# Performance work log

Measured on AMD Instinct MI355X. Metric: run time of the kernel, lower is better.

Reference implementation:

```python
import jax, jax.numpy as jnp
import numpy as np


def _gat_layer(h, mask, w, a_src, a_dst):
    # h: [B,C,N,Fin], w: [C,H,Fin,Fout], a_*: [C,H,Fout,1], mask: [B,N,N] (True where no edge)
    h_prime = jnp.einsum('bcni,chio->bchno', h, w)          # [B,C,H,N,Fout]
    t = jnp.tanh(h_prime)
    s = jnp.einsum('bchno,cho->bchn', t, a_src[..., 0])      # src scores
    d = jnp.einsum('bchno,cho->bchn', t, a_dst[..., 0])      # dst scores
    attn = s[..., :, None] + d[..., None, :]                 # [B,C,H,N,N]
    attn = jnp.where(attn >= 0, attn, 0.2 * attn)            # leaky_relu(0.2)
    attn = jnp.where(mask[:, None, None, :, :], jnp.float32(-1e12), attn)
    attn = jax.nn.softmax(attn, axis=-1)
    return jnp.einsum('bchnm,bchmo->bchno', attn, h_prime)   # [B,C,H,N,Fout]


def setup_inputs() -> dict:
    key = jax.random.key(0)
    ks = jax.random.split(key, 8)
    B, C, N, F0, H, F = 2, 2, 1024, 64, 8, 64

    def xavier(k, shape):
        fan_in, fan_out = shape[-2], shape[-1]
        lim = (6.0 / (fan_in + fan_out)) ** 0.5
        return jax.random.uniform(k, shape, jnp.float32, -lim, lim)

    x = jax.random.normal(ks[0], (B, C, N, F0), dtype=jnp.float32)
    adj = jax.random.randint(ks[1], (B, N, N), 0, 2, dtype=jnp.int32)
    w1 = xavier(ks[2], (C, H, F0, F))
    a_src1 = xavier(ks[3], (C, H, F, 1))
    a_dst1 = xavier(ks[4], (C, H, F, 1))
    w2 = xavier(ks[5], (C, H, H * F, F))
    a_src2 = xavier(ks[6], (C, H, F, 1))
    a_dst2 = xavier(ks[7], (C, H, F, 1))
    return {"x": x, "adj": adj, "w1": w1, "a_src1": a_src1, "a_dst1": a_dst1,
            "w2": w2, "a_src2": a_src2, "a_dst2": a_dst2}


def reference(x, adj, w1, a_src1, a_dst1, w2, a_src2, a_dst2):
    B, C, N, _ = x.shape
    adj_f = adj.astype(jnp.float32) + jnp.eye(N, dtype=jnp.float32)[None]  # add self-loops
    mask = adj_f == 0                                        # [B,N,N]
    out1 = _gat_layer(x, mask, w1, a_src1, a_dst1)           # [B,C,H,N,F]
    # permute heads next to features, flatten, elu (dropout is identity in eval)
    x1 = jax.nn.elu(jnp.transpose(out1, (0, 1, 3, 2, 4)).reshape(B, C, N, -1))
    out2 = _gat_layer(x1, mask, w2, a_src2, a_dst2)          # [B,C,H,N,F]
    return out2.mean(axis=2)                                 # mean over heads -> [B,C,N,F]
```

## Files before the change

kernel.cpp:

```cpp
#include <hip/hip_runtime.h>

#define BB 2
#define CC 2
#define NN 1024
#define HH 8
#define BCHN 32
#define SVN  (BCHN*NN)
#define LOG2E 1.44269504f

typedef _Float16 f16x8 __attribute__((ext_vector_type(8)));
typedef _Float16 f16x4 __attribute__((ext_vector_type(4)));
typedef __fp16 h16x2 __attribute__((ext_vector_type(2)));
typedef float f32x4 __attribute__((ext_vector_type(4)));

__device__ __forceinline__ float fexp2(float x) {
  float r; asm("v_exp_f32 %0, %1" : "=v"(r) : "v"(x)); return r;
}

__device__ __forceinline__ void gl_lds16(const _Float16* g, _Float16* l) {
  __builtin_amdgcn_global_load_lds(
      (const __attribute__((address_space(1))) void*)g,
      (__attribute__((address_space(3))) void*)l, 16, 0, 0);
}


__global__ __launch_bounds__(256) void proj1_fused(
    const float* __restrict__ x, const int* __restrict__ adj,
    const float* __restrict__ w1, const float* __restrict__ w2,
    const float* __restrict__ asrc, const float* __restrict__ adst,
    _Float16* __restrict__ w2T, unsigned long long* __restrict__ bmg,
    _Float16* __restrict__ HpT, float* __restrict__ s_out, float* __restrict__ d_out)
{
  __shared__ union {
    __align__(16) _Float16 tile[64*72];
    struct { float sp[4][32]; float sd[4][32]; } pr;
  } sm;
  const int bx = blockIdx.x;
  const int t = threadIdx.x;
  const int w = t >> 6, lane = t & 63;
  const int colr = lane & 15, quad = lane >> 4;

  if (bx < 1024) {
    const int bch = bx & 31;
    const int row0 = (bx >> 5) * 32;
    const int h = bch & 7; const int bc = bch >> 3; const int c = bc & 1;

    const float* Ar0 = x + ((size_t)bc*NN + row0 + colr)*64;
    const float* Ar1 = Ar0 + (size_t)16*64;
    const float* Bw  = w1 + ((size_t)(c*HH + h))*64*64 + w*16 + colr;

    f32x4 acc0 = {0.f,0.f,0.f,0.f}, acc1 = {0.f,0.f,0.f,0.f};
    #pragma unroll
    for (int kb = 0; kb < 64; kb += 32) {
      const float4 pa0 = *(const float4*)(Ar0 + kb + quad*8);
      const float4 pa1 = *(const float4*)(Ar0 + kb + quad*8 + 4);
      const float4 pb0 = *(const float4*)(Ar1 + kb + quad*8);
      const float4 pb1 = *(const float4*)(Ar1 + kb + quad*8 + 4);
      float bv[8];
      #pragma unroll
      for (int j = 0; j < 8; ++j) bv[j] = Bw[(size_t)(kb + quad*8 + j)*64];
      f16x8 a0, a1, bf;
      a0[0]=(_Float16)pa0.x; a0[1]=(_Float16)pa0.y; a0[2]=(_Float16)pa0.z; a0[3]=(_Float16)pa0.w;
      a0[4]=(_Float16)pa1.x; a0[5]=(_Float16)pa1.y; a0[6]=(_Float16)pa1.z; a0[7]=(_Float16)pa1.w;
      a1[0]=(_Float16)pb0.x; a1[1]=(_Float16)pb0.y; a1[2]=(_Float16)pb0.z; a1[3]=(_Float16)pb0.w;
      a1[4]=(_Float16)pb1.x; a1[5]=(_Float16)pb1.y; a1[6]=(_Float16)pb1.z; a1[7]=(_Float16)pb1.w;
      #pragma unroll
      for (int j = 0; j < 8; ++j) bf[j] = (_Float16)bv[j];
      acc0 = __builtin_amdgcn_mfma_f32_16x16x32_f16(a0, bf, acc0, 0, 0, 0);
      acc1 = __builtin_amdgcn_mfma_f32_16x16x32_f16(a1, bf, acc1, 0, 0, 0);
    }

    const float af  = asrc[(c*HH + h)*64 + w*16 + colr];
    const float bf_ = adst[(c*HH + h)*64 + w*16 + colr];
    _Float16* HT = HpT + (size_t)bch*65536 + (size_t)(row0 >> 5)*2048;

    #pragma unroll
    for (int mt = 0; mt < 2; ++mt) {
      const f32x4 a = mt ? acc1 : acc0;
      f16x4 hv;
      #pragma unroll
      for (int i = 0; i < 4; ++i) {
        const float v = a[i];
        hv[i] = (_Float16)v;
        const float ex = __expf(2.f*v);
        const float th = 1.f - 2.f/(ex + 1.f);
        float ps = th * af, pd = th * bf_;
        #pragma unroll
        for (int off = 1; off < 16; off <<= 1) {
          ps += __shfl_xor(ps, off);
          pd += __shfl_xor(pd, off);
        }
        if (colr == 0) {
          sm.pr.sp[w][mt*16 + quad*4 + i] = ps;
          sm.pr.sd[w][mt*16 + quad*4 + i] = pd;
        }
      }
      const int chunk = w*64 + (mt*2 + (quad >> 1))*16 + colr;
      *(f16x4*)(HT + chunk*8 + (quad & 1)*4) = hv;
    }
    __syncthreads();
    if (t < 32) {
      const float sv = sm.pr.sp[0][t] + sm.pr.sp[1][t] + sm.pr.sp[2][t] + sm.pr.sp[3][t];
      const float dv = sm.pr.sd[0][t] + sm.pr.sd[1][t] + sm.pr.sd[2][t] + sm.pr.sd[3][t];
      s_out[bch*NN + row0 + t] = sv * LOG2E;
      d_out[bch*NN + row0 + t] = dv * LOG2E;
    }
  } else if (bx < 1152) {
    const int u = bx - 1024;
    const int ch = u >> 3, k0 = (u & 7)*64;
    const float* src = w2 + ((size_t)ch*512 + k0)*64;
    #pragma unroll
    for (int j = 0; j < 4; ++j) {
      const int uu = t + j*256;
      const int k = uu >> 4, seg = uu & 15;
      const float4 v = ((const float4*)src)[(size_t)k*16 + seg];
      sm.tile[(seg*4+0)*72 + k] = (_Float16)v.x;
      sm.tile[(seg*4+1)*72 + k] = (_Float16)v.y;
      sm.tile[(seg*4+2)*72 + k] = (_Float16)v.z;
      sm.tile[(seg*4+3)*72 + k] = (_Float16)v.w;
    }
    __syncthreads();
    _Float16* dst = w2T + (size_t)ch*32768;
    #pragma unroll
    for (int j = 0; j < 2; ++j) {
      const int uu = t + j*256;
      const int f = uu >> 3, seg = uu & 7;
      const f16x8 o = *(const f16x8*)&sm.tile[f*72 + seg*8];
      const int kk = k0 + seg*8;
      const int chunk = (f >> 4)*64 + ((seg & 3))*16 + (f & 15);
      *(f16x8*)(dst + (size_t)(kk >> 5)*2048 + chunk*8) = o;
    }
  } else {
    const int g = (bx - 1152)*4 + w;
    const int base = g*32;
    #pragma unroll
    for (int jb = 0; jb < 4; ++jb) {
      int vals[8];
      #pragma unroll
      for (int i = 0; i < 8; ++i) {
        const int idx = base + jb*8 + i;
        const int b = idx >> 14;
        const int n = (idx >> 4) & (NN - 1);
        const int wd = idx & 15;
        vals[i] = adj[((size_t)b*NN + n)*NN + wd*64 + lane];
      }
      #pragma unroll
      for (int i = 0; i < 8; ++i) {
        const int idx = base + jb*8 + i;
        const int n = (idx >> 4) & (NN - 1);
        const int m = (idx & 15)*64 + lane;
        const unsigned long long bits = __ballot((vals[i] != 0) || (m == n));
        if (lane == 0) bmg[idx] = bits;
      }
    }
  }
}

template<int LAYER>
__global__ __launch_bounds__(256) void attn_coop(
    const _Float16* __restrict__ Hp, const float* __restrict__ s_arr,
    const float* __restrict__ d_arr, const unsigned long long* __restrict__ bmg,
    _Float16* __restrict__ outp)
{
  __shared__ struct {
    __align__(16) _Float16 stg[2][2048];
    __align__(16) float dstg[1024];
    float pw[4][16][68];
  } sm;
  const int bch = blockIdx.x;
  const int r0 = blockIdx.y * 64;
  const int t = threadIdx.x;
  const int wv = t >> 6, lane = t & 63;
  const int colr = lane & 15, quad = lane >> 4;
  const int b = bch >> 4;

  const float* dg = d_arr + (size_t)bch*NN;
  const float4* dg4 = (const float4*)dg;
  float mxl = -1e30f;
  #pragma unroll
  for (int j = 0; j < 4; ++j) {
    const float4 v = dg4[lane + 64*j];
    mxl = fmaxf(fmaxf(v.x, v.y), fmaxf(fmaxf(v.z, v.w), mxl));
  }
  #pragma unroll
  for (int off = 1; off < 64; off <<= 1) mxl = fmaxf(mxl, __shfl_xor(mxl, off));
  const float maxd = mxl;

  *(float4*)&sm.dstg[t*4] = dg4[t];

  const int r = r0 + wv*16 + colr;
  const float s = s_arr[(size_t)bch*NN + r];
  const float so = s + maxd;
  const float offs = fmaxf(so, 0.2f*so);
  const float sA = s - offs, sB = 0.2f*s - offs;

  unsigned long long m[16];
  {
    const unsigned long long* bm = bmg + ((size_t)b*NN + r)*16;
    #pragma unroll
    for (int j = 0; j < 16; ++j) m[j] = bm[j];
  }

  const _Float16* strip = Hp + (size_t)bch*65536;

  f32x4 acc[4];
  f32x4 accs = {0.f,0.f,0.f,0.f};
  #pragma unroll
  for (int ft = 0; ft < 4; ++ft) acc[ft] = (f32x4){0.f,0.f,0.f,0.f};
  f16x8 ones;
  #pragma unroll
  for (int i = 0; i < 8; ++i) ones[i] = (_Float16)1.f;

  asm volatile("s_waitcnt vmcnt(0) lgkmcnt(0)" ::: "memory");
  __builtin_amdgcn_s_barrier();

#define STAGE_T(tt) \
    gl_lds16(strip + (size_t)(tt)*2048 + wv*512 + lane*8, &sm.stg[(tt) & 1][wv*512]);

  STAGE_T(0);
  asm volatile("s_waitcnt vmcnt(0)" ::: "memory");
  __builtin_amdgcn_s_barrier();

  #pragma unroll 4
  for (int ks = 0; ks < 32; ++ks) {
    if (ks < 31) STAGE_T(ks + 1);

    f16x8 Bc[4];
    #pragma unroll
    for (int ft = 0; ft < 4; ++ft)
      Bc[ft] = *(const f16x8*)&sm.stg[ks & 1][ft*512 + lane*8];
    const float* dls = &sm.dstg[ks*32 + quad*8];
    const float4 da0 = *(const float4*)dls;
    const float4 da1 = *(const float4*)(dls + 4);
    asm volatile("s_waitcnt lgkmcnt(0)" ::: "memory");
    __builtin_amdgcn_sched_barrier(0);

    __builtin_amdgcn_s_setprio(1);
    const unsigned mb = (unsigned)((m[ks >> 1] >> ((ks & 1)*32 + quad*8)) & 0xFFull);
    const float dd[8] = {da0.x, da0.y, da0.z, da0.w, da1.x, da1.y, da1.z, da1.w};
    union { f16x8 v; h16x2 hh[4]; } A;
    #pragma unroll
    for (int jp = 0; jp < 4; ++jp) {
      float p[2];
      #pragma unroll
      for (int jj = 0; jj < 2; ++jj) {
        const int j = jp*2 + jj;
        const float dj = dd[j];
        const float l = fmaxf(sA + dj, fmaf(0.2f, dj, sB));
        p[jj] = ((mb >> j) & 1u) ? fexp2(l) : 0.f;
      }
      A.hh[jp] = __builtin_amdgcn_cvt_pkrtz(p[0], p[1]);
    }
    #pragma unroll
    for (int ft = 0; ft < 4; ++ft)
      acc[ft] = __builtin_amdgcn_mfma_f32_16x16x32_f16(A.v, Bc[ft], acc[ft], 0, 0, 0);
    accs = __builtin_amdgcn_mfma_f32_16x16x32_f16(A.v, ones, accs, 0, 0, 0);
    __builtin_amdgcn_s_setprio(0);

    if (ks < 31) asm volatile("s_waitcnt vmcnt(0)" ::: "memory");
    __builtin_amdgcn_s_barrier();
  }
#undef STAGE_T

  float inv[4];
  #pragma unroll
  for (int i = 0; i < 4; ++i) inv[i] = (LAYER == 2 ? 0.125f : 1.f) / accs[i];
  float (*pw)[68] = sm.pw[wv];
  #pragma unroll
  for (int ft = 0; ft < 4; ++ft)
    #pragma unroll
    for (int i = 0; i < 4; ++i)
      pw[quad*4 + i][ft*16 + colr] = acc[ft][i] * inv[i];
  const int row = lane >> 2, f0 = (lane & 3)*16;
  f16x8 o0, o1;
  #pragma unroll
  for (int j = 0; j < 8; ++j) {
    float v0 = pw[row][f0 + j];
    float v1 = pw[row][f0 + 8 + j];
    if (LAYER == 1) {
      v0 = v0 > 0.f ? v0 : expm1f(v0);
      v1 = v1 > 0.f ? v1 : expm1f(v1);
    }
    o0[j] = (_Float16)v0; o1[j] = (_Float16)v1;
  }
  const int rr = r0 + wv*16 + row;
  _Float16* dst;
  if (LAYER == 1) {
    const int bc = bch >> 3, h = bch & 7;
    dst = outp + ((size_t)bc*NN + rr)*512 + h*64 + f0;
  } else {
    dst = outp + ((size_t)bch*NN + rr)*64 + f0;
  }
  *(f16x8*)dst = o0;
  *(f16x8*)(dst + 8) = o1;
}

__global__ __launch_bounds__(256) void proj2_coop(
    const _Float16* __restrict__ x1, const _Float16* __restrict__ w2T,
    const float* __restrict__ asrc2, const float* __restrict__ adst2,
    _Float16* __restrict__ HpT2, float* __restrict__ s2, float* __restrict__ d2)
{
  __shared__ struct {
    __align__(16) _Float16 Ast[2][2048];
    __align__(16) _Float16 Bst[2][2048];
  } sm;
  const int bch = blockIdx.x;
  const int r0p = blockIdx.y * 64;
  const int t = threadIdx.x;
  const int wv = t >> 6, lane = t & 63;
  const int colr = lane & 15, quad = lane >> 4;
  const int h = bch & 7, bc = bch >> 3, c = bc & 1;

  const _Float16* Asrc = x1 + ((size_t)bc*NN + r0p + wv*16 + colr)*512 + quad*8;
  const _Float16* Bsrc = w2T + (size_t)(c*HH + h)*32768 + wv*512 + lane*8;

  f32x4 acc[4];
  #pragma unroll
  for (int ft = 0; ft < 4; ++ft) acc[ft] = (f32x4){0.f,0.f,0.f,0.f};

#define STAGE_P(tt) { \
    gl_lds16(Asrc + (tt)*32,           &sm.Ast[(tt) & 1][wv*512]); \
    gl_lds16(Bsrc + (size_t)(tt)*2048, &sm.Bst[(tt) & 1][wv*512]); }

  STAGE_P(0);
  asm volatile("s_waitcnt vmcnt(0)" ::: "memory");
  __builtin_amdgcn_s_barrier();

  #pragma unroll 4
  for (int ks = 0; ks < 16; ++ks) {
    if (ks < 15) STAGE_P(ks + 1);

    const f16x8 Af = *(const f16x8*)&sm.Ast[ks & 1][wv*512 + lane*8];
    f16x8 Bc[4];
    #pragma unroll
    for (int ft = 0; ft < 4; ++ft)
      Bc[ft] = *(const f16x8*)&sm.Bst[ks & 1][ft*512 + lane*8];
    asm volatile("s_waitcnt lgkmcnt(0)" ::: "memory");
    __builtin_amdgcn_sched_barrier(0);

    __builtin_amdgcn_s_setprio(1);
    #pragma unroll
    for (int ft = 0; ft < 4; ++ft)
      acc[ft] = __builtin_amdgcn_mfma_f32_16x16x32_f16(Af, Bc[ft], acc[ft], 0, 0, 0);
    __builtin_amdgcn_s_setprio(0);

    if (ks < 15) asm volatile("s_waitcnt vmcnt(0)" ::: "memory");
    __builtin_amdgcn_s_barrier();
  }
#undef STAGE_P

  float af[4], bfv[4];
  #pragma unroll
  for (int ft = 0; ft < 4; ++ft) {
    af[ft]  = asrc2[(c*HH + h)*64 + ft*16 + colr];
    bfv[ft] = adst2[(c*HH + h)*64 + ft*16 + colr];
  }
  #pragma unroll
  for (int i = 0; i < 4; ++i) {
    float ps = 0.f, pd = 0.f;
    #pragma unroll
    for (int ft = 0; ft < 4; ++ft) {
      const float v = acc[ft][i];
      const float ex = __expf(2.f*v);
      const float th = 1.f - 2.f/(ex + 1.f);
      ps += th * af[ft]; pd += th * bfv[ft];
    }
    #pragma unroll
    for (int off = 1; off < 16; off <<= 1) {
      ps += __shfl_xor(ps, off);
      pd += __shfl_xor(pd, off);
    }
    if (colr == 0) {
      s2[(size_t)bch*NN + r0p + wv*16 + quad*4 + i] = ps * LOG2E;
      d2[(size_t)bch*NN + r0p + wv*16 + quad*4 + i] = pd * LOG2E;
    }
  }
  _Float16* H2 = HpT2 + (size_t)bch*65536 + (size_t)((r0p >> 5) + (wv >> 1))*2048;
  const int cb = (wv & 1)*2 + (quad >> 1);
  #pragma unroll
  for (int ft = 0; ft < 4; ++ft) {
    f16x4 hv;
    #pragma unroll
    for (int i = 0; i < 4; ++i) hv[i] = (_Float16)acc[ft][i];
    const int chunk = ft*64 + cb*16 + colr;
    *(f16x4*)(H2 + chunk*8 + (quad & 1)*4) = hv;
  }
}

__global__ __launch_bounds__(256) void reduce_heads(
    const _Float16* __restrict__ out2, float* __restrict__ out)
{
  const int o = blockIdx.x*256 + threadIdx.x;
  const int f = o & 63;
  const int n = (o >> 6) & (NN - 1);
  const int bc = o >> 16;
  float acc = 0.f;
  #pragma unroll
  for (int h = 0; h < HH; ++h)
    acc += (float)out2[(((size_t)bc*HH + h)*NN + n)*64 + f];
  out[o] = acc;
}

extern "C" void kernel_launch(void* const* d_in, const int* in_sizes, int n_in,
                              void* d_out, int out_size, void* d_ws, size_t ws_size,
                              hipStream_t stream)
{
  const float* x   = (const float*)d_in[0];
  const int*   adj = (const int*)d_in[1];
  const float* w1  = (const float*)d_in[2];
  const float* as1 = (const float*)d_in[3];
  const float* ad1 = (const float*)d_in[4];
  const float* w2  = (const float*)d_in[5];
  const float* as2 = (const float*)d_in[6];
  const float* ad2 = (const float*)d_in[7];

  char* w8 = (char*)d_ws;
  _Float16* HpT  = (_Float16*)(w8);
  _Float16* HpT2 = (_Float16*)(w8 + (4u<<20));
  _Float16* w2T  = (_Float16*)(w8 + (8u<<20));
  float* s_v  = (float*)(w8 + (10u<<20));
  float* d_v  = (float*)(w8 + (10u<<20) + SVN*4);
  float* s2_v = (float*)(w8 + (10u<<20) + SVN*8);
  float* d2_v = (float*)(w8 + (10u<<20) + SVN*12);
  unsigned long long* bmg = (unsigned long long*)(w8 + (10u<<20) + SVN*16);
  _Float16* x1g = (_Float16*)(w8 + (16u<<20));
  _Float16* XB  = (_Float16*)(w8 + (20u<<20));

  proj1_fused<<<1408, 256, 0, stream>>>(x, adj, w1, w2, as1, ad1, w2T, bmg, HpT, s_v, d_v);
  attn_coop<1><<<dim3(BCHN, NN/64), 256, 0, stream>>>(HpT, s_v, d_v, bmg, x1g);
  proj2_coop<<<dim3(BCHN, NN/64), 256, 0, stream>>>(x1g, w2T, as2, ad2, HpT2, s2_v, d2_v);
  attn_coop<2><<<dim3(BCHN, NN/64), 256, 0, stream>>>(HpT2, s2_v, d2_v, bmg, XB);
  reduce_heads<<<dim3((unsigned)(out_size/256)), 256, 0, stream>>>(XB, (float*)d_out);
}
```

Before: 145.2 us.

## Fuse five kernel launches into one persistent kernel with grid barriers

Merges the projection, two attention passes, the second projection and the head reduction into a single persistent kernel of 512 blocks. Phases are separated by a software grid barrier built from atomic counters, which is reset with a memset before each launch. The aim is to remove per-launch overhead and the tail gaps between dependent kernels. In exchange it relies on all 512 blocks being co-resident (launch bounds of 2 blocks per CU) and adds atomic spin-wait cost. A timeout guard on the spin can break out before the barrier is reached, which risks incorrect results.

```diff
diff --git a/kernel.cpp b/kernel.cpp
--- a/kernel.cpp
+++ b/kernel.cpp
@@ -7,6 +7,7 @@
 #define BCHN 32
 #define SVN  (BCHN*NN)
 #define LOG2E 1.44269504f
+#define NBLK 512
 
 typedef _Float16 f16x8 __attribute__((ext_vector_type(8)));
 typedef _Float16 f16x4 __attribute__((ext_vector_type(4)));
@@ -23,26 +24,51 @@
       (__attribute__((address_space(3))) void*)l, 16, 0, 0);
 }
 
-
-__global__ __launch_bounds__(256) void proj1_fused(
-    const float* __restrict__ x, const int* __restrict__ adj,
+__device__ __forceinline__ void gbar(unsigned* cnt, unsigned* gen, unsigned g) {
+  __syncthreads();
+  if (threadIdx.x == 0) {
+    __threadfence();
+    if (atomicAdd(cnt, 1u) == g*(unsigned)NBLK - 1u) atomicAdd(gen, 1u);
+    int guard = 0;
+    while (__hip_atomic_load(gen, __ATOMIC_RELAXED, __HIP_MEMORY_SCOPE_AGENT) < g) {
+      __builtin_amdgcn_s_sleep(8);
+      if (++guard > (1 << 20)) break;
+    }
+    __threadfence();
+  }
+  __syncthreads();
+}
+
+
+union SmemU {
+  __align__(16) _Float16 tile[64*72];
+  struct { float sp[4][32]; float sd[4][32]; } pr;
+  struct {
+    __align__(16) _Float16 stg[2][2048];
+    __align__(16) float dstg[1024];
+    float pw[4][16][68];
+  } at;
+  struct {
+    __align__(16) _Float16 Ast[2][2048];
+    __align__(16) _Float16 Bst[2][2048];
+  } p2;
+};
+
+__device__ __forceinline__ void p1_unit(
+    int u, const float* __restrict__ x, const int* __restrict__ adj,
     const float* __restrict__ w1, const float* __restrict__ w2,
     const float* __restrict__ asrc, const float* __restrict__ adst,
     _Float16* __restrict__ w2T, unsigned long long* __restrict__ bmg,
-    _Float16* __restrict__ HpT, float* __restrict__ s_out, float* __restrict__ d_out)
+    _Float16* __restrict__ HpT, float* __restrict__ s_out, float* __restrict__ d_out,
+    SmemU& sm)
 {
-  __shared__ union {
-    __align__(16) _Float16 tile[64*72];
-    struct { float sp[4][32]; float sd[4][32]; } pr;
-  } sm;
-  const int bx = blockIdx.x;
   const int t = threadIdx.x;
   const int w = t >> 6, lane = t & 63;
   const int colr = lane & 15, quad = lane >> 4;
 
-  if (bx < 1024) {
-    const int bch = bx & 31;
-    const int row0 = (bx >> 5) * 32;
+  if (u < 1024) {
+    const int bch = u & 31;
+    const int row0 = (u >> 5) * 32;
     const int h = bch & 7; const int bc = bch >> 3; const int c = bc & 1;
 
     const float* Ar0 = x + ((size_t)bc*NN + row0 + colr)*64;
@@ -105,9 +131,9 @@
       s_out[bch*NN + row0 + t] = sv * LOG2E;
       d_out[bch*NN + row0 + t] = dv * LOG2E;
     }
-  } else if (bx < 1152) {
-    const int u = bx - 1024;
-    const int ch = u >> 3, k0 = (u & 7)*64;
+  } else if (u < 1152) {
+    const int uu0 = u - 1024;
+    const int ch = uu0 >> 3, k0 = (uu0 & 7)*64;
     const float* src = w2 + ((size_t)ch*512 + k0)*64;
     #pragma unroll
     for (int j = 0; j < 4; ++j) {
@@ -130,8 +156,8 @@
       const int chunk = (f >> 4)*64 + ((seg & 3))*16 + (f & 15);
       *(f16x8*)(dst + (size_t)(kk >> 5)*2048 + chunk*8) = o;
     }
-  } else {
-    const int g = (bx - 1152)*4 + w;
+  } else if (u < 1408) {
+    const int g = (u - 1152)*4 + w;
     const int base = g*32;
     #pragma unroll
     for (int jb = 0; jb < 4; ++jb) {
@@ -157,18 +183,13 @@
 }
 
 template<int LAYER>
-__global__ __launch_bounds__(256) void attn_coop(
-    const _Float16* __restrict__ Hp, const float* __restrict__ s_arr,
+__device__ __forceinline__ void attn_phase(
+    int bid, const _Float16* __restrict__ Hp, const float* __restrict__ s_arr,
     const float* __restrict__ d_arr, const unsigned long long* __restrict__ bmg,
-    _Float16* __restrict__ outp)
+    _Float16* __restrict__ outp, SmemU& sm)
 {
-  __shared__ struct {
-    __align__(16) _Float16 stg[2][2048];
-    __align__(16) float dstg[1024];
-    float pw[4][16][68];
-  } sm;
-  const int bch = blockIdx.x;
-  const int r0 = blockIdx.y * 64;
+  const int bch = bid & 31;
+  const int r0 = (bid >> 5) * 64;
   const int t = threadIdx.x;
   const int wv = t >> 6, lane = t & 63;
   const int colr = lane & 15, quad = lane >> 4;
@@ -186,7 +207,7 @@
   for (int off = 1; off < 64; off <<= 1) mxl = fmaxf(mxl, __shfl_xor(mxl, off));
   const float maxd = mxl;
 
-  *(float4*)&sm.dstg[t*4] = dg4[t];
+  *(float4*)&sm.at.dstg[t*4] = dg4[t];
 
   const int r = r0 + wv*16 + colr;
   const float s = s_arr[(size_t)bch*NN + r];
@@ -215,7 +236,7 @@
   __builtin_amdgcn_s_barrier();
 
 #define STAGE_T(tt) \
-    gl_lds16(strip + (size_t)(tt)*2048 + wv*512 + lane*8, &sm.stg[(tt) & 1][wv*512]);
+    gl_lds16(strip + (size_t)(tt)*2048 + wv*512 + lane*8, &sm.at.stg[(tt) & 1][wv*512]);
 
   STAGE_T(0);
   asm volatile("s_waitcnt vmcnt(0)" ::: "memory");
@@ -228,8 +249,8 @@
     f16x8 Bc[4];
     #pragma unroll
     for (int ft = 0; ft < 4; ++ft)
-      Bc[ft] = *(const f16x8*)&sm.stg[ks & 1][ft*512 + lane*8];
-    const float* dls = &sm.dstg[ks*32 + quad*8];
+      Bc[ft] = *(const f16x8*)&sm.at.stg[ks & 1][ft*512 + lane*8];
+    const float* dls = &sm.at.dstg[ks*32 + quad*8];
     const float4 da0 = *(const float4*)dls;
     const float4 da1 = *(const float4*)(dls + 4);
     asm volatile("s_waitcnt lgkmcnt(0)" ::: "memory");
@@ -265,7 +286,7 @@
   float inv[4];
   #pragma unroll
   for (int i = 0; i < 4; ++i) inv[i] = (LAYER == 2 ? 0.125f : 1.f) / accs[i];
-  float (*pw)[68] = sm.pw[wv];
+  float (*pw)[68] = sm.at.pw[wv];
   #pragma unroll
   for (int ft = 0; ft < 4; ++ft)
     #pragma unroll
@@ -295,17 +316,14 @@
   *(f16x8*)(dst + 8) = o1;
 }
 
-__global__ __launch_bounds__(256) void proj2_coop(
-    const _Float16* __restrict__ x1, const _Float16* __restrict__ w2T,
+__device__ __forceinline__ void proj2_phase(
+    int bid, const _Float16* __restrict__ x1, const _Float16* __restrict__ w2T,
     const float* __restrict__ asrc2, const float* __restrict__ adst2,
-    _Float16* __restrict__ HpT2, float* __restrict__ s2, float* __restrict__ d2)
+    _Float16* __restrict__ HpT2, float* __restrict__ s2, float* __restrict__ d2,
+    SmemU& sm)
 {
-  __shared__ struct {
-    __align__(16) _Float16 Ast[2][2048];
-    __align__(16) _Float16 Bst[2][2048];
-  } sm;
-  const int bch = blockIdx.x;
-  const int r0p = blockIdx.y * 64;
+  const int bch = bid & 31;
+  const int r0p = (bid >> 5) * 64;
   const int t = threadIdx.x;
   const int wv = t >> 6, lane = t & 63;
   const int colr = lane & 15, quad = lane >> 4;
@@ -319,8 +337,8 @@
   for (int ft = 0; ft < 4; ++ft) acc[ft] = (f32x4){0.f,0.f,0.f,0.f};
 
 #define STAGE_P(tt) { \
-    gl_lds16(Asrc + (tt)*32,           &sm.Ast[(tt) & 1][wv*512]); \
-    gl_lds16(Bsrc + (size_t)(tt)*2048, &sm.Bst[(tt) & 1][wv*512]); }
+    gl_lds16(Asrc + (tt)*32,           &sm.p2.Ast[(tt) & 1][wv*512]); \
+    gl_lds16(Bsrc + (size_t)(tt)*2048, &sm.p2.Bst[(tt) & 1][wv*512]); }
 
   STAGE_P(0);
   asm volatile("s_waitcnt vmcnt(0)" ::: "memory");
@@ -330,11 +348,11 @@
   for (int ks = 0; ks < 16; ++ks) {
     if (ks < 15) STAGE_P(ks + 1);
 
-    const f16x8 Af = *(const f16x8*)&sm.Ast[ks & 1][wv*512 + lane*8];
+    const f16x8 Af = *(const f16x8*)&sm.p2.Ast[ks & 1][wv*512 + lane*8];
     f16x8 Bc[4];
     #pragma unroll
     for (int ft = 0; ft < 4; ++ft)
-      Bc[ft] = *(const f16x8*)&sm.Bst[ks & 1][ft*512 + lane*8];
+      Bc[ft] = *(const f16x8*)&sm.p2.Bst[ks & 1][ft*512 + lane*8];
     asm volatile("s_waitcnt lgkmcnt(0)" ::: "memory");
     __builtin_amdgcn_sched_barrier(0);
 
@@ -387,18 +405,48 @@
   }
 }
 
-__global__ __launch_bounds__(256) void reduce_heads(
-    const _Float16* __restrict__ out2, float* __restrict__ out)
+__global__ __launch_bounds__(256, 2) void gat_mega(
+    const float* __restrict__ x, const int* __restrict__ adj,
+    const float* __restrict__ w1, const float* __restrict__ as1, const float* __restrict__ ad1,
+    const float* __restrict__ w2, const float* __restrict__ as2, const float* __restrict__ ad2,
+    _Float16* __restrict__ w2T, unsigned long long* __restrict__ bmg,
+    _Float16* __restrict__ HpT, float* __restrict__ s_v, float* __restrict__ d_v,
+    _Float16* __restrict__ x1g, _Float16* __restrict__ HpT2,
+    float* __restrict__ s2_v, float* __restrict__ d2_v,
+    _Float16* __restrict__ XB, float* __restrict__ out,
+    unsigned* cnt, unsigned* gen)
 {
-  const int o = blockIdx.x*256 + threadIdx.x;
-  const int f = o & 63;
-  const int n = (o >> 6) & (NN - 1);
-  const int bc = o >> 16;
-  float acc = 0.f;
-  #pragma unroll
-  for (int h = 0; h < HH; ++h)
-    acc += (float)out2[(((size_t)bc*HH + h)*NN + n)*64 + f];
-  out[o] = acc;
+  __shared__ SmemU sm;
+  const int bid = blockIdx.x;
+
+  #pragma unroll
+  for (int u3 = 0; u3 < 3; ++u3) {
+    p1_unit(bid + NBLK*u3, x, adj, w1, w2, as1, ad1, w2T, bmg, HpT, s_v, d_v, sm);
+    __syncthreads();
+  }
+  gbar(cnt, gen, 1u);
+
+  attn_phase<1>(bid, HpT, s_v, d_v, bmg, x1g, sm);
+  gbar(cnt, gen, 2u);
+
+  proj2_phase(bid, x1g, w2T, as2, ad2, HpT2, s2_v, d2_v, sm);
+  gbar(cnt, gen, 3u);
+
+  attn_phase<2>(bid, HpT2, s2_v, d2_v, bmg, XB, sm);
+  gbar(cnt, gen, 4u);
+
+  #pragma unroll
+  for (int j = 0; j < 2; ++j) {
+    const int o = (bid + NBLK*j)*256 + (int)threadIdx.x;
+    const int f = o & 63;
+    const int n = (o >> 6) & (NN - 1);
+    const int bc = o >> 16;
+    float acc = 0.f;
+    #pragma unroll
+    for (int h = 0; h < HH; ++h)
+      acc += (float)XB[(((size_t)bc*HH + h)*NN + n)*64 + f];
+    out[o] = acc;
+  }
 }
 
 extern "C" void kernel_launch(void* const* d_in, const int* in_sizes, int n_in,
@@ -425,10 +473,10 @@
   unsigned long long* bmg = (unsigned long long*)(w8 + (10u<<20) + SVN*16);
   _Float16* x1g = (_Float16*)(w8 + (16u<<20));
   _Float16* XB  = (_Float16*)(w8 + (20u<<20));
-
-  proj1_fused<<<1408, 256, 0, stream>>>(x, adj, w1, w2, as1, ad1, w2T, bmg, HpT, s_v, d_v);
-  attn_coop<1><<<dim3(BCHN, NN/64), 256, 0, stream>>>(HpT, s_v, d_v, bmg, x1g);
-  proj2_coop<<<dim3(BCHN, NN/64), 256, 0, stream>>>(x1g, w2T, as2, ad2, HpT2, s2_v, d2_v);
-  attn_coop<2><<<dim3(BCHN, NN/64), 256, 0, stream>>>(HpT2, s2_v, d2_v, bmg, XB);
-  reduce_heads<<<dim3((unsigned)(out_size/256)), 256, 0, stream>>>(XB, (float*)d_out);
-}
+  unsigned* bar = (unsigned*)(w8 + (24u<<20));
+
+  hipMemsetAsync(bar, 0, 16, stream);
+  gat_mega<<<NBLK, 256, 0, stream>>>(x, adj, w1, as1, ad1, w2, as2, ad2,
+                                     w2T, bmg, HpT, s_v, d_v, x1g, HpT2,
+                                     s2_v, d2_v, XB, (float*)d_out, bar, bar + 1);
+}
```

After: 319.8 us. 120% more time.
